# Kernel optimization log

Measured on AMD Instinct MI355X. Metric: run time of the kernel, lower is better.

Reference implementation:

```python
import jax, jax.numpy as jnp
import numpy as np


def setup_inputs() -> dict:
    key = jax.random.key(0)
    ks = jax.random.split(key, 5)
    B, S, D, H, K = 2, 2048, 1024, 16, 64
    std = 0.02
    return {
        "x": jax.random.normal(ks[0], (B, S, D), dtype=jnp.float32),
        "W_Q": jax.random.normal(ks[1], (H, D, K), dtype=jnp.float32) * std,
        "W_K": jax.random.normal(ks[2], (H, D, K), dtype=jnp.float32) * std,
        "W_V": jax.random.normal(ks[3], (H, D, K), dtype=jnp.float32) * std,
        "W_O": jax.random.normal(ks[4], (H, K, D), dtype=jnp.float32) * std,
        "b_Q": jnp.zeros((H, K), dtype=jnp.float32),
        "b_K": jnp.zeros((H, K), dtype=jnp.float32),
        "b_V": jnp.zeros((H, K), dtype=jnp.float32),
        "b_O": jnp.zeros((D,), dtype=jnp.float32),
    }


def reference(x, W_Q, W_K, W_V, W_O, b_Q, b_K, b_V, b_O):
    # x: (B, S, D); W_*: (H, D, K); W_O: (H, K, D)
    S = x.shape[1]
    d_head = W_Q.shape[-1]
    q = jnp.einsum('bpd,hdk->bphk', x, W_Q) + b_Q
    k = jnp.einsum('bpd,hdk->bphk', x, W_K) + b_K
    v = jnp.einsum('bpd,hdk->bphk', x, W_V) + b_V
    scores = jnp.einsum('bphk,bqhk->bhpq', q, k) / jnp.sqrt(jnp.float32(d_head))
    # causal mask: positions q > p (strict upper triangle) are masked
    causal = jnp.tril(jnp.ones((S, S), dtype=bool))
    scores = jnp.where(causal, scores, jnp.float32(-jnp.inf))
    pattern = jax.nn.softmax(scores, axis=-1)
    z = jnp.einsum('bhpq,bqhk->bphk', pattern, v)
    out = jnp.einsum('bphk,hkd->bpd', z, W_O) + b_O
    return out
```

## Files before the change

### kernel.cpp

```cpp
#include <hip/hip_runtime.h>

typedef unsigned short u16;
typedef __attribute__((ext_vector_type(4))) float f32x4;
typedef __attribute__((ext_vector_type(8))) short s16x8;
typedef __attribute__((ext_vector_type(4))) unsigned short u16x4;
typedef __attribute__((ext_vector_type(2))) unsigned int u32x2;

#define S_ 2048
#define D_ 1024
#define H_ 16
#define KH 64
#define M_ 4096
#define BH_ 32

__device__ __forceinline__ float bf2f(u16 v) {
    union { unsigned int u; float f; } x; x.u = ((unsigned int)v) << 16; return x.f;
}
__device__ __forceinline__ u16 f2bf(float f) {
    union { float ff; unsigned int u; } x; x.ff = f;
    unsigned int r = x.u + 0x7fffu + ((x.u >> 16) & 1u);
    return (u16)(r >> 16);
}
__device__ __forceinline__ unsigned int cvt_pk_bf16(float lo, float hi) {
    unsigned int d;
    asm("v_cvt_pk_bf16_f32 %0, %1, %2" : "=v"(d) : "v"(lo), "v"(hi));
    return d;
}

__global__ void kcvt_x(const float* __restrict__ x, u16* __restrict__ xb) {
    const int i = (blockIdx.x * 256 + threadIdx.x) * 4;
    const float4 v = *(const float4*)&x[i];
    u16x4 o;
    o.x = f2bf(v.x); o.y = f2bf(v.y); o.z = f2bf(v.z); o.w = f2bf(v.w);
    *(u16x4*)&xb[i] = o;
}

__global__ void ktrans_w(const float* __restrict__ WQ, const float* __restrict__ WK,
                         const float* __restrict__ WV, const float* __restrict__ WO,
                         u16* __restrict__ wt) {
    __shared__ u16 tile[64][65];
    const int mat = blockIdx.z;
    const float* src = (mat == 0) ? WQ : (mat == 1) ? WK : (mat == 2) ? WV : WO;
    u16* dst = wt + (size_t)mat * 1048576;
    const int a0 = blockIdx.x * 64, b0 = blockIdx.y * 64;
    const int t = threadIdx.x;
    const int bl = t & 63, ar = t >> 6;
    #pragma unroll
    for (int i = 0; i < 16; ++i) {
        int a = a0 + i * 4 + ar, b = b0 + bl;
        size_t sa = (mat < 3) ? (((size_t)(b >> 6)) << 16) + ((size_t)a << 6) + (b & 63)
                              : (size_t)a * 1024 + b;
        tile[i * 4 + ar][bl] = f2bf(src[sa]);
    }
    __syncthreads();
    #pragma unroll
    for (int i = 0; i < 16; ++i) {
        int bl2 = i * 4 + ar;
        dst[(size_t)(b0 + bl2) * 1024 + a0 + bl] = tile[bl][bl2];
    }
}

__global__ __launch_bounds__(256)
void kgemm0(const u16* __restrict__ A, const u16* __restrict__ Wt,
            const float* __restrict__ b0p, const float* __restrict__ b1p,
            const float* __restrict__ b2p,
            u16* __restrict__ Qo, u16* __restrict__ Ko, u16* __restrict__ Vto) {
    __shared__ u16 As[2][128 * 32];
    __shared__ u16 Bs[2][128 * 32];
    const int t = threadIdx.x;
    const int l = t & 63, w = t >> 6;
    const int lq = l & 15, lg = l >> 4;
    const int wr = w >> 1, wc = w & 1;
    const int m0 = blockIdx.x * 128;
    const int n0 = blockIdx.y * 128;
    const int z = blockIdx.z;
    const u16* Bt = Wt + (size_t)z * 1048576;
    const float* bias = (z == 0) ? b0p : (z == 1) ? b1p : b2p;

    f32x4 acc[4][4] = {};

    auto stage = [&](int kt, int buf) {
        #pragma unroll
        for (int i = 0; i < 2; ++i) {
            int idx = t + i * 256;
            int row = idx >> 2, cc = idx & 3;
            const u16* ga = A + (size_t)(m0 + row) * 1024 + kt * 32 + cc * 8;
            const u16* gb = Bt + (size_t)(n0 + row) * 1024 + kt * 32 + cc * 8;
            __builtin_amdgcn_global_load_lds(
                (const __attribute__((address_space(1))) unsigned int*)ga,
                (__attribute__((address_space(3))) unsigned int*)(&As[buf][idx * 8]),
                16, 0, 0);
            __builtin_amdgcn_global_load_lds(
                (const __attribute__((address_space(1))) unsigned int*)gb,
                (__attribute__((address_space(3))) unsigned int*)(&Bs[buf][idx * 8]),
                16, 0, 0);
        }
    };

    stage(0, 0);
    __syncthreads();
    for (int kt = 0; kt < 32; ++kt) {
        const int cur = kt & 1;
        if (kt + 1 < 32) stage(kt + 1, cur ^ 1);
        s16x8 af[4], bf[4];
        #pragma unroll
        for (int m = 0; m < 4; ++m)
            af[m] = *(const s16x8*)&As[cur][(wr * 64 + m * 16 + lq) * 32 + lg * 8];
        #pragma unroll
        for (int n = 0; n < 4; ++n)
            bf[n] = *(const s16x8*)&Bs[cur][(wc * 64 + n * 16 + lq) * 32 + lg * 8];
        #pragma unroll
        for (int m = 0; m < 4; ++m)
            #pragma unroll
            for (int n = 0; n < 4; ++n)
                acc[m][n] = __builtin_amdgcn_mfma_f32_16x16x32_bf16(
                    bf[n], af[m], acc[m][n], 0, 0, 0);
        __syncthreads();
    }

    #pragma unroll
    for (int n = 0; n < 4; ++n) {
        const int gcolb = n0 + wc * 64 + n * 16 + lg * 4;
        const float4 bv = *(const float4*)&bias[gcolb];
        const int h = gcolb >> 6, kk0 = gcolb & 63;
        #pragma unroll
        for (int m = 0; m < 4; ++m) {
            const int grow = m0 + wr * 64 + m * 16 + lq;
            const int b = grow >> 11, s = grow & 2047;
            const float v0 = acc[m][n][0] + bv.x;
            const float v1 = acc[m][n][1] + bv.y;
            const float v2 = acc[m][n][2] + bv.z;
            const float v3 = acc[m][n][3] + bv.w;
            if (z == 2) {
                u16* vb = Vto + ((size_t)((b * 16 + h) * 64 + kk0) * 2048 + s);
                vb[0] = f2bf(v0); vb[2048] = f2bf(v1);
                vb[4096] = f2bf(v2); vb[6144] = f2bf(v3);
            } else {
                u16* outp = (z == 0) ? Qo : Ko;
                u32x2 wp;
                wp.x = cvt_pk_bf16(v0, v1);
                wp.y = cvt_pk_bf16(v2, v3);
                *(u32x2*)&outp[((size_t)(b * 16 + h) * 2048 + s) * 64 + kk0] = wp;
            }
        }
    }
}

__global__ __launch_bounds__(256)
void kgemm1(const u16* __restrict__ A, const u16* __restrict__ Bt,
            const float* __restrict__ bias, float* __restrict__ fo) {
    __shared__ u16 As[2][128 * 32];
    __shared__ u16 Bs[2][64 * 32];
    const int t = threadIdx.x;
    const int l = t & 63, w = t >> 6;
    const int lq = l & 15, lg = l >> 4;
    const int wr = w >> 1, wc = w & 1;
    const int m0 = blockIdx.x * 128;
    const int n0 = blockIdx.y * 64;

    f32x4 acc[4][2] = {};

    auto stage = [&](int kt, int buf) {
        #pragma unroll
        for (int i = 0; i < 2; ++i) {
            int idx = t + i * 256;
            int row = idx >> 2, cc = idx & 3;
            __builtin_amdgcn_global_load_lds(
                (const __attribute__((address_space(1))) unsigned int*)
                    (A + (size_t)(m0 + row) * 1024 + kt * 32 + cc * 8),
                (__attribute__((address_space(3))) unsigned int*)(&As[buf][idx * 8]),
                16, 0, 0);
        }
        {
            int row = t >> 2, cc = t & 3;
            __builtin_amdgcn_global_load_lds(
                (const __attribute__((address_space(1))) unsigned int*)
                    (Bt + (size_t)(n0 + row) * 1024 + kt * 32 + cc * 8),
                (__attribute__((address_space(3))) unsigned int*)(&Bs[buf][t * 8]),
                16, 0, 0);
        }
    };

    stage(0, 0);
    __syncthreads();
    for (int kt = 0; kt < 32; ++kt) {
        const int cur = kt & 1;
        if (kt + 1 < 32) stage(kt + 1, cur ^ 1);
        s16x8 af[4], bf[2];
        #pragma unroll
        for (int m = 0; m < 4; ++m)
            af[m] = *(const s16x8*)&As[cur][(wr * 64 + m * 16 + lq) * 32 + lg * 8];
        #pragma unroll
        for (int n = 0; n < 2; ++n)
            bf[n] = *(const s16x8*)&Bs[cur][(wc * 32 + n * 16 + lq) * 32 + lg * 8];
        #pragma unroll
        for (int m = 0; m < 4; ++m)
            #pragma unroll
            for (int n = 0; n < 2; ++n)
                acc[m][n] = __builtin_amdgcn_mfma_f32_16x16x32_bf16(
                    bf[n], af[m], acc[m][n], 0, 0, 0);
        __syncthreads();
    }

    #pragma unroll
    for (int n = 0; n < 2; ++n) {
        const int gcolb = n0 + wc * 32 + n * 16 + lg * 4;
        const float4 bv = *(const float4*)&bias[gcolb];
        #pragma unroll
        for (int m = 0; m < 4; ++m) {
            const int grow = m0 + wr * 64 + m * 16 + lq;
            float4 o;
            o.x = acc[m][n][0] + bv.x;
            o.y = acc[m][n][1] + bv.y;
            o.z = acc[m][n][2] + bv.z;
            o.w = acc[m][n][3] + bv.w;
            *(float4*)&fo[(size_t)grow * 1024 + gcolb] = o;
        }
    }
}

__global__ __launch_bounds__(256)
void kattn(const u16* __restrict__ Q, const u16* __restrict__ K,
           const u16* __restrict__ Vt, u16* __restrict__ Z) {
    __shared__ u16 Ks[2][64 * 64];
    __shared__ u16 Vs[2][64 * 64];
    __shared__ u16 Pl[4][16 * 72];
    const int t = threadIdx.x, l = t & 63, w = t >> 6;
    const int lq = l & 15, lg = l >> 4;

    const int lin = blockIdx.x + 16 * blockIdx.y;
    const int xcd = lin & 7;
    const int idx = lin >> 3;
    const int pair = idx & 15;
    const int bh = xcd + 8 * (idx >> 4);

    const size_t base = (size_t)bh * (S_ * KH);
    const u16* Qb = Q + base;
    const u16* Kb = K + base;
    const u16* Vb = Vt + base;
    const int b = bh >> 4, h = bh & 15;
    u16* Pw = &Pl[w][0];

    const int c0 = ((lg ^ (lq & 7)) * 8);
    const int c1 = c0 ^ 32;
    const float NINF = -__builtin_inff();

    auto stage = [&](int k0, int buf) {
        #pragma unroll
        for (int i = 0; i < 2; ++i) {
            const int idx2 = t + i * 256;
            const int row = idx2 >> 3;
            const int cg = (idx2 & 7) ^ (row & 7);
            __builtin_amdgcn_global_load_lds(
                (const __attribute__((address_space(1))) unsigned int*)
                    (Kb + (size_t)(k0 + row) * KH + cg * 8),
                (__attribute__((address_space(3))) unsigned int*)(&Ks[buf][idx2 * 8]),
                16, 0, 0);
            __builtin_amdgcn_global_load_lds(
                (const __attribute__((address_space(1))) unsigned int*)
                    (Vb + (size_t)row * S_ + k0 + cg * 8),
                (__attribute__((address_space(3))) unsigned int*)(&Vs[buf][idx2 * 8]),
                16, 0, 0);
        }
    };

    const float SCL = 0.18033688011112042f;

    #pragma unroll 1
    for (int ph = 0; ph < 2; ++ph) {
        const int qt = ph ? (31 - pair) : pair;
        const int nt = qt + 1;
        const int qs = qt * 64 + w * 16;
        const int lim = w * 16 + lq;

        const s16x8 qf0 = *(const s16x8*)&Qb[(size_t)(qs + lq) * KH + lg * 8];
        const s16x8 qf1 = *(const s16x8*)&Qb[(size_t)(qs + lq) * KH + 32 + lg * 8];

        float mrow = NINF, lrow = 0.f;
        f32x4 zacc[4] = {};

        stage(0, 0);
        __syncthreads();

        for (int kt = 0; kt < nt; ++kt) {
            const int buf = kt & 1;
            if (kt + 1 < nt) stage((kt + 1) * 64, buf ^ 1);

            f32x4 sf[4] = {};
            __builtin_amdgcn_s_setprio(1);
            #pragma unroll
            for (int kf = 0; kf < 4; ++kf) {
                const int row = kf * 16 + lq;
                const s16x8 ka = *(const s16x8*)&Ks[buf][row * 64 + c0];
                const s16x8 kb = *(const s16x8*)&Ks[buf][row * 64 + c1];
                sf[kf] = __builtin_amdgcn_mfma_f32_16x16x32_bf16(ka, qf0, sf[kf], 0, 0, 0);
                sf[kf] = __builtin_amdgcn_mfma_f32_16x16x32_bf16(kb, qf1, sf[kf], 0, 0, 0);
            }
            __builtin_amdgcn_s_setprio(0);

            float p[4][4];
            const bool diag = (kt == qt);
            #pragma unroll
            for (int kf = 0; kf < 4; ++kf)
                #pragma unroll
                for (int r = 0; r < 4; ++r) {
                    float v = sf[kf][r] * SCL;
                    if (diag && (kf * 16 + lg * 4 + r) > lim) v = NINF;
                    p[kf][r] = v;
                }

            float mk[4];
            #pragma unroll
            for (int kf = 0; kf < 4; ++kf)
                mk[kf] = fmaxf(fmaxf(p[kf][0], p[kf][1]), fmaxf(p[kf][2], p[kf][3]));
            float tmax = fmaxf(fmaxf(mk[0], mk[1]), fmaxf(mk[2], mk[3]));
            tmax = fmaxf(tmax, __shfl_xor(tmax, 16));
            tmax = fmaxf(tmax, __shfl_xor(tmax, 32));

            float alpha = 1.f;
            if (!__all(tmax <= mrow + 8.f)) {
                const float nm = fmaxf(mrow, tmax);
                alpha = exp2f(mrow - nm);
                mrow = nm;
                #pragma unroll
                for (int nf = 0; nf < 4; ++nf)
                    #pragma unroll
                    for (int r = 0; r < 4; ++r)
                        zacc[nf][r] *= alpha;
            }

            float sk[4];
            #pragma unroll
            for (int kf = 0; kf < 4; ++kf) {
                #pragma unroll
                for (int r = 0; r < 4; ++r)
                    p[kf][r] = exp2f(p[kf][r] - mrow);
                sk[kf] = (p[kf][0] + p[kf][1]) + (p[kf][2] + p[kf][3]);
            }
            float rsum = (sk[0] + sk[1]) + (sk[2] + sk[3]);
            rsum += __shfl_xor(rsum, 16);
            rsum += __shfl_xor(rsum, 32);
            lrow = lrow * alpha + rsum;

            #pragma unroll
            for (int kf = 0; kf < 4; ++kf) {
                u32x2 wp;
                wp.x = cvt_pk_bf16(p[kf][0], p[kf][1]);
                wp.y = cvt_pk_bf16(p[kf][2], p[kf][3]);
                *(u32x2*)&Pw[lq * 72 + kf * 16 + lg * 4] = wp;
            }
            const s16x8 pa0 = *(const s16x8*)&Pw[lq * 72 + lg * 8];
            const s16x8 pa1 = *(const s16x8*)&Pw[lq * 72 + 32 + lg * 8];

            __builtin_amdgcn_s_setprio(1);
            #pragma unroll
            for (int nf = 0; nf < 4; ++nf) {
                const int row = nf * 16 + lq;
                const s16x8 v0 = *(const s16x8*)&Vs[buf][row * 64 + c0];
                const s16x8 v1 = *(const s16x8*)&Vs[buf][row * 64 + c1];
                zacc[nf] = __builtin_amdgcn_mfma_f32_16x16x32_bf16(v0, pa0, zacc[nf], 0, 0, 0);
                zacc[nf] = __builtin_amdgcn_mfma_f32_16x16x32_bf16(v1, pa1, zacc[nf], 0, 0, 0);
            }
            __builtin_amdgcn_s_setprio(0);
            __syncthreads();
        }

        const float rinv = 1.f / lrow;
        const size_t zrow = (size_t)(b * S_ + qs + lq) * 1024 + h * 64;
        #pragma unroll
        for (int nf = 0; nf < 4; ++nf) {
            u32x2 wp;
            wp.x = cvt_pk_bf16(zacc[nf][0] * rinv, zacc[nf][1] * rinv);
            wp.y = cvt_pk_bf16(zacc[nf][2] * rinv, zacc[nf][3] * rinv);
            *(u32x2*)&Z[zrow + nf * 16 + lg * 4] = wp;
        }
    }
}

extern "C" void kernel_launch(void* const* d_in, const int* in_sizes, int n_in,
                              void* d_out, int out_size, void* d_ws, size_t ws_size,
                              hipStream_t stream) {
    const float* x  = (const float*)d_in[0];
    const float* WQ = (const float*)d_in[1];
    const float* WK = (const float*)d_in[2];
    const float* WV = (const float*)d_in[3];
    const float* WO = (const float*)d_in[4];
    const float* bQ = (const float*)d_in[5];
    const float* bK = (const float*)d_in[6];
    const float* bV = (const float*)d_in[7];
    const float* bO = (const float*)d_in[8];
    float* out = (float*)d_out;

    u16* ws  = (u16*)d_ws;
    u16* xb  = ws;
    u16* wt  = xb + 4194304u;
    u16* Qb  = wt + 4194304u;
    u16* Kb  = Qb + 4194304u;
    u16* Vtb = Kb + 4194304u;
    u16* Zb  = Vtb + 4194304u;

    kcvt_x<<<dim3(4096), 256, 0, stream>>>(x, xb);
    ktrans_w<<<dim3(16, 16, 4), 256, 0, stream>>>(WQ, WK, WV, WO, wt);
    kgemm0<<<dim3(32, 8, 3), 256, 0, stream>>>(
        xb, wt, bQ, bK, bV, Qb, Kb, Vtb);
    kattn<<<dim3(16, BH_), 256, 0, stream>>>(Qb, Kb, Vtb, Zb);
    kgemm1<<<dim3(32, 16), 256, 0, stream>>>(
        Zb, wt + 3u * 1048576u, bO, out);
}
```

Baseline: 206.5 us.

## Software-pipeline QK^T into the previous step and vectorize V-transpose stores

The attention loop now computes the next tile's QK^T scores right after the barrier at the end of the current step, using ping-pong score registers, so the MFMA work for tile kt+1 can overlap the softmax of tile kt. Separately, the projection GEMM swaps MFMA operand order for the V output so each lane holds four consecutive sequence positions. That lets the transposed V store be one packed 8-byte write instead of four scalar 2-byte writes. The cost is extra registers for the second score buffer, which may reduce occupancy.

```diff
diff --git a/kernel.cpp b/kernel.cpp
--- a/kernel.cpp
+++ b/kernel.cpp
@@ -109,37 +109,54 @@
         #pragma unroll
         for (int n = 0; n < 4; ++n)
             bf[n] = *(const s16x8*)&Bs[cur][(wc * 64 + n * 16 + lq) * 32 + lg * 8];
-        #pragma unroll
-        for (int m = 0; m < 4; ++m)
-            #pragma unroll
-            for (int n = 0; n < 4; ++n)
-                acc[m][n] = __builtin_amdgcn_mfma_f32_16x16x32_bf16(
-                    bf[n], af[m], acc[m][n], 0, 0, 0);
+        if (z == 2) {
+            #pragma unroll
+            for (int m = 0; m < 4; ++m)
+                #pragma unroll
+                for (int n = 0; n < 4; ++n)
+                    acc[m][n] = __builtin_amdgcn_mfma_f32_16x16x32_bf16(
+                        af[m], bf[n], acc[m][n], 0, 0, 0);
+        } else {
+            #pragma unroll
+            for (int m = 0; m < 4; ++m)
+                #pragma unroll
+                for (int n = 0; n < 4; ++n)
+                    acc[m][n] = __builtin_amdgcn_mfma_f32_16x16x32_bf16(
+                        bf[n], af[m], acc[m][n], 0, 0, 0);
+        }
         __syncthreads();
     }
 
-    #pragma unroll
-    for (int n = 0; n < 4; ++n) {
-        const int gcolb = n0 + wc * 64 + n * 16 + lg * 4;
-        const float4 bv = *(const float4*)&bias[gcolb];
-        const int h = gcolb >> 6, kk0 = gcolb & 63;
-        #pragma unroll
-        for (int m = 0; m < 4; ++m) {
-            const int grow = m0 + wr * 64 + m * 16 + lq;
-            const int b = grow >> 11, s = grow & 2047;
-            const float v0 = acc[m][n][0] + bv.x;
-            const float v1 = acc[m][n][1] + bv.y;
-            const float v2 = acc[m][n][2] + bv.z;
-            const float v3 = acc[m][n][3] + bv.w;
-            if (z == 2) {
-                u16* vb = Vto + ((size_t)((b * 16 + h) * 64 + kk0) * 2048 + s);
-                vb[0] = f2bf(v0); vb[2048] = f2bf(v1);
-                vb[4096] = f2bf(v2); vb[6144] = f2bf(v3);
-            } else {
-                u16* outp = (z == 0) ? Qo : Ko;
+    if (z == 2) {
+        #pragma unroll
+        for (int n = 0; n < 4; ++n) {
+            const int gcol = n0 + wc * 64 + n * 16 + lq;
+            const float bv = bias[gcol];
+            const int h = gcol >> 6, kk = gcol & 63;
+            #pragma unroll
+            for (int m = 0; m < 4; ++m) {
+                const int growb = m0 + wr * 64 + m * 16 + lg * 4;
+                const int b = growb >> 11, s = growb & 2047;
                 u32x2 wp;
-                wp.x = cvt_pk_bf16(v0, v1);
-                wp.y = cvt_pk_bf16(v2, v3);
+                wp.x = cvt_pk_bf16(acc[m][n][0] + bv, acc[m][n][1] + bv);
+                wp.y = cvt_pk_bf16(acc[m][n][2] + bv, acc[m][n][3] + bv);
+                *(u32x2*)&Vto[(size_t)((b * 16 + h) * 64 + kk) * 2048 + s] = wp;
+            }
+        }
+    } else {
+        u16* outp = (z == 0) ? Qo : Ko;
+        #pragma unroll
+        for (int n = 0; n < 4; ++n) {
+            const int gcolb = n0 + wc * 64 + n * 16 + lg * 4;
+            const float4 bv = *(const float4*)&bias[gcolb];
+            const int h = gcolb >> 6, kk0 = gcolb & 63;
+            #pragma unroll
+            for (int m = 0; m < 4; ++m) {
+                const int grow = m0 + wr * 64 + m * 16 + lq;
+                const int b = grow >> 11, s = grow & 2047;
+                u32x2 wp;
+                wp.x = cvt_pk_bf16(acc[m][n][0] + bv.x, acc[m][n][1] + bv.y);
+                wp.y = cvt_pk_bf16(acc[m][n][2] + bv.z, acc[m][n][3] + bv.w);
                 *(u32x2*)&outp[((size_t)(b * 16 + h) * 2048 + s) * 64 + kk0] = wp;
             }
         }
@@ -244,6 +261,7 @@
     const int c0 = ((lg ^ (lq & 7)) * 8);
     const int c1 = c0 ^ 32;
     const float NINF = -__builtin_inff();
+    const float SCL = 0.18033688011112042f;
 
     auto stage = [&](int k0, int buf) {
         #pragma unroll
@@ -263,8 +281,6 @@
                 16, 0, 0);
         }
     };
-
-    const float SCL = 0.18033688011112042f;
 
     #pragma unroll 1
     for (int ph = 0; ph < 2; ++ph) {
@@ -278,25 +294,26 @@
 
         float mrow = NINF, lrow = 0.f;
         f32x4 zacc[4] = {};
-
-        stage(0, 0);
-        __syncthreads();
-
-        for (int kt = 0; kt < nt; ++kt) {
-            const int buf = kt & 1;
-            if (kt + 1 < nt) stage((kt + 1) * 64, buf ^ 1);
-
-            f32x4 sf[4] = {};
+        f32x4 sfA[4], sfB[4];
+
+        auto QK = [&](int buf, f32x4 (&sfo)[4]) {
             __builtin_amdgcn_s_setprio(1);
             #pragma unroll
             for (int kf = 0; kf < 4; ++kf) {
                 const int row = kf * 16 + lq;
                 const s16x8 ka = *(const s16x8*)&Ks[buf][row * 64 + c0];
                 const s16x8 kb = *(const s16x8*)&Ks[buf][row * 64 + c1];
-                sf[kf] = __builtin_amdgcn_mfma_f32_16x16x32_bf16(ka, qf0, sf[kf], 0, 0, 0);
-                sf[kf] = __builtin_amdgcn_mfma_f32_16x16x32_bf16(kb, qf1, sf[kf], 0, 0, 0);
+                f32x4 z4 = {};
+                z4 = __builtin_amdgcn_mfma_f32_16x16x32_bf16(ka, qf0, z4, 0, 0, 0);
+                sfo[kf] = __builtin_amdgcn_mfma_f32_16x16x32_bf16(kb, qf1, z4, 0, 0, 0);
             }
             __builtin_amdgcn_s_setprio(0);
+        };
+
+        auto STEP = [&](f32x4 (&sfc)[4], f32x4 (&sfn)[4], int kt) {
+            const int buf = kt & 1;
+            const bool hn = (kt + 1 < nt);
+            if (hn) stage((kt + 1) * 64, buf ^ 1);
 
             float p[4][4];
             const bool diag = (kt == qt);
@@ -304,7 +321,7 @@
             for (int kf = 0; kf < 4; ++kf)
                 #pragma unroll
                 for (int r = 0; r < 4; ++r) {
-                    float v = sf[kf][r] * SCL;
+                    float v = sfc[kf][r] * SCL;
                     if (diag && (kf * 16 + lg * 4 + r) > lim) v = NINF;
                     p[kf][r] = v;
                 }
@@ -363,6 +380,15 @@
             }
             __builtin_amdgcn_s_setprio(0);
             __syncthreads();
+            if (hn) QK(buf ^ 1, sfn);
+        };
+
+        stage(0, 0);
+        __syncthreads();
+        QK(0, sfA);
+        for (int kt = 0; kt < nt; kt += 2) {
+            STEP(sfA, sfB, kt);
+            if (kt + 1 < nt) STEP(sfB, sfA, kt + 1);
         }
 
         const float rinv = 1.f / lrow;
```

Measured after the change: 238.0 us. 15.3% more time.

## Split V projection into transposed-MFMA kernel and remap output GEMM blocks per XCD

Applied to the files above, without the earlier changes.

The QKV projection is split in two. Q and K keep the old kernel, while V gets a template variant that swaps the MFMA operands. The accumulator then holds consecutive sequence positions per lane, so the transposed V store becomes packed 8-byte writes instead of scattered 2-byte stores. The output projection GEMM also switches to a 1D grid with an XCD-aware block mapping so blocks sharing A rows land on the same die's L2. The cost is an extra kernel launch, and the smaller V-only grid may underfill the GPU.

```diff
diff --git a/kernel.cpp b/kernel.cpp
--- a/kernel.cpp
+++ b/kernel.cpp
@@ -60,11 +60,11 @@
     }
 }
 
+template <int VM>
 __global__ __launch_bounds__(256)
-void kgemm0(const u16* __restrict__ A, const u16* __restrict__ Wt,
-            const float* __restrict__ b0p, const float* __restrict__ b1p,
-            const float* __restrict__ b2p,
-            u16* __restrict__ Qo, u16* __restrict__ Ko, u16* __restrict__ Vto) {
+void kgemm0t(const u16* __restrict__ A, const u16* __restrict__ Wt,
+             const float* __restrict__ b0p, const float* __restrict__ b1p,
+             u16* __restrict__ o0, u16* __restrict__ o1) {
     __shared__ u16 As[2][128 * 32];
     __shared__ u16 Bs[2][128 * 32];
     const int t = threadIdx.x;
@@ -73,9 +73,10 @@
     const int wr = w >> 1, wc = w & 1;
     const int m0 = blockIdx.x * 128;
     const int n0 = blockIdx.y * 128;
-    const int z = blockIdx.z;
+    const int z = (VM == 0) ? blockIdx.z : 0;
     const u16* Bt = Wt + (size_t)z * 1048576;
-    const float* bias = (z == 0) ? b0p : (z == 1) ? b1p : b2p;
+    const float* bias = z ? b1p : b0p;
+    u16* outp = z ? o1 : o0;
 
     f32x4 acc[4][4] = {};
 
@@ -112,34 +113,46 @@
         #pragma unroll
         for (int m = 0; m < 4; ++m)
             #pragma unroll
-            for (int n = 0; n < 4; ++n)
-                acc[m][n] = __builtin_amdgcn_mfma_f32_16x16x32_bf16(
-                    bf[n], af[m], acc[m][n], 0, 0, 0);
+            for (int n = 0; n < 4; ++n) {
+                if constexpr (VM == 1)
+                    acc[m][n] = __builtin_amdgcn_mfma_f32_16x16x32_bf16(
+                        af[m], bf[n], acc[m][n], 0, 0, 0);
+                else
+                    acc[m][n] = __builtin_amdgcn_mfma_f32_16x16x32_bf16(
+                        bf[n], af[m], acc[m][n], 0, 0, 0);
+            }
         __syncthreads();
     }
 
-    #pragma unroll
-    for (int n = 0; n < 4; ++n) {
-        const int gcolb = n0 + wc * 64 + n * 16 + lg * 4;
-        const float4 bv = *(const float4*)&bias[gcolb];
-        const int h = gcolb >> 6, kk0 = gcolb & 63;
-        #pragma unroll
-        for (int m = 0; m < 4; ++m) {
-            const int grow = m0 + wr * 64 + m * 16 + lq;
-            const int b = grow >> 11, s = grow & 2047;
-            const float v0 = acc[m][n][0] + bv.x;
-            const float v1 = acc[m][n][1] + bv.y;
-            const float v2 = acc[m][n][2] + bv.z;
-            const float v3 = acc[m][n][3] + bv.w;
-            if (z == 2) {
-                u16* vb = Vto + ((size_t)((b * 16 + h) * 64 + kk0) * 2048 + s);
-                vb[0] = f2bf(v0); vb[2048] = f2bf(v1);
-                vb[4096] = f2bf(v2); vb[6144] = f2bf(v3);
-            } else {
-                u16* outp = (z == 0) ? Qo : Ko;
+    if constexpr (VM == 1) {
+        #pragma unroll
+        for (int n = 0; n < 4; ++n) {
+            const int gcol = n0 + wc * 64 + n * 16 + lq;
+            const float bv = bias[gcol];
+            const int h = gcol >> 6, kk = gcol & 63;
+            #pragma unroll
+            for (int m = 0; m < 4; ++m) {
+                const int growb = m0 + wr * 64 + m * 16 + lg * 4;
+                const int b = growb >> 11, s = growb & 2047;
                 u32x2 wp;
-                wp.x = cvt_pk_bf16(v0, v1);
-                wp.y = cvt_pk_bf16(v2, v3);
+                wp.x = cvt_pk_bf16(acc[m][n][0] + bv, acc[m][n][1] + bv);
+                wp.y = cvt_pk_bf16(acc[m][n][2] + bv, acc[m][n][3] + bv);
+                *(u32x2*)&o0[(size_t)((b * 16 + h) * 64 + kk) * 2048 + s] = wp;
+            }
+        }
+    } else {
+        #pragma unroll
+        for (int n = 0; n < 4; ++n) {
+            const int gcolb = n0 + wc * 64 + n * 16 + lg * 4;
+            const float4 bv = *(const float4*)&bias[gcolb];
+            const int h = gcolb >> 6, kk0 = gcolb & 63;
+            #pragma unroll
+            for (int m = 0; m < 4; ++m) {
+                const int grow = m0 + wr * 64 + m * 16 + lq;
+                const int b = grow >> 11, s = grow & 2047;
+                u32x2 wp;
+                wp.x = cvt_pk_bf16(acc[m][n][0] + bv.x, acc[m][n][1] + bv.y);
+                wp.y = cvt_pk_bf16(acc[m][n][2] + bv.z, acc[m][n][3] + bv.w);
                 *(u32x2*)&outp[((size_t)(b * 16 + h) * 2048 + s) * 64 + kk0] = wp;
             }
         }
@@ -155,8 +168,14 @@
     const int l = t & 63, w = t >> 6;
     const int lq = l & 15, lg = l >> 4;
     const int wr = w >> 1, wc = w & 1;
-    const int m0 = blockIdx.x * 128;
-    const int n0 = blockIdx.y * 64;
+
+    const int lin = blockIdx.x;
+    const int xcd = lin & 7;
+    const int s = lin >> 3;
+    const int nb = s & 15;
+    const int mb = (s >> 4) * 8 + xcd;
+    const int m0 = mb * 128;
+    const int n0 = nb * 64;
 
     f32x4 acc[4][2] = {};
 
@@ -401,9 +420,10 @@
 
     kcvt_x<<<dim3(4096), 256, 0, stream>>>(x, xb);
     ktrans_w<<<dim3(16, 16, 4), 256, 0, stream>>>(WQ, WK, WV, WO, wt);
-    kgemm0<<<dim3(32, 8, 3), 256, 0, stream>>>(
-        xb, wt, bQ, bK, bV, Qb, Kb, Vtb);
+    kgemm0t<0><<<dim3(32, 8, 2), 256, 0, stream>>>(xb, wt, bQ, bK, Qb, Kb);
+    kgemm0t<1><<<dim3(32, 8, 1), 256, 0, stream>>>(
+        xb, wt + 2u * 1048576u, bV, nullptr, Vtb, nullptr);
     kattn<<<dim3(16, BH_), 256, 0, stream>>>(Qb, Kb, Vtb, Zb);
-    kgemm1<<<dim3(32, 16), 256, 0, stream>>>(
+    kgemm1<<<dim3(512), 256, 0, stream>>>(
         Zb, wt + 3u * 1048576u, bO, out);
 }
```

Result: slower. 223.0 us (+8.0%).

## Launch one attention block per q-tile longest-first, XCD-aware swizzle for output GEMM

Applied to the files above, without the earlier changes.

Each attention block now handles a single 64-row query tile instead of a balanced pair, giving 1024 blocks ordered so the longest causal tiles are dispatched first. Block indices are mapped so blocks sharing a batch-head land on the same XCD. The output projection GEMM gets a 1D grid with an XCD-aware mapping so blocks reading the same A rows share an XCD's L2. This trades the paired-tile load balancing for more, smaller blocks and relies on the dispatch order to keep the tail short.

```diff
diff --git a/kernel.cpp b/kernel.cpp
--- a/kernel.cpp
+++ b/kernel.cpp
@@ -155,8 +155,14 @@
     const int l = t & 63, w = t >> 6;
     const int lq = l & 15, lg = l >> 4;
     const int wr = w >> 1, wc = w & 1;
-    const int m0 = blockIdx.x * 128;
-    const int n0 = blockIdx.y * 64;
+
+    const int lin = blockIdx.x;
+    const int xcd = lin & 7;
+    const int s = lin >> 3;
+    const int nb = s & 15;
+    const int mb = (s >> 4) * 8 + xcd;
+    const int m0 = mb * 128;
+    const int n0 = nb * 64;
 
     f32x4 acc[4][2] = {};
 
@@ -228,11 +234,11 @@
     const int t = threadIdx.x, l = t & 63, w = t >> 6;
     const int lq = l & 15, lg = l >> 4;
 
-    const int lin = blockIdx.x + 16 * blockIdx.y;
+    const int lin = blockIdx.x;
     const int xcd = lin & 7;
-    const int idx = lin >> 3;
-    const int pair = idx & 15;
-    const int bh = xcd + 8 * (idx >> 4);
+    const int r = lin >> 3;
+    const int qt = 31 - (r >> 2);
+    const int bh = xcd + 8 * (r & 3);
 
     const size_t base = (size_t)bh * (S_ * KH);
     const u16* Qb = Q + base;
@@ -244,6 +250,7 @@
     const int c0 = ((lg ^ (lq & 7)) * 8);
     const int c1 = c0 ^ 32;
     const float NINF = -__builtin_inff();
+    const float SCL = 0.18033688011112042f;
 
     auto stage = [&](int k0, int buf) {
         #pragma unroll
@@ -264,116 +271,110 @@
         }
     };
 
-    const float SCL = 0.18033688011112042f;
-
-    #pragma unroll 1
-    for (int ph = 0; ph < 2; ++ph) {
-        const int qt = ph ? (31 - pair) : pair;
-        const int nt = qt + 1;
-        const int qs = qt * 64 + w * 16;
-        const int lim = w * 16 + lq;
-
-        const s16x8 qf0 = *(const s16x8*)&Qb[(size_t)(qs + lq) * KH + lg * 8];
-        const s16x8 qf1 = *(const s16x8*)&Qb[(size_t)(qs + lq) * KH + 32 + lg * 8];
-
-        float mrow = NINF, lrow = 0.f;
-        f32x4 zacc[4] = {};
-
-        stage(0, 0);
+    const int nt = qt + 1;
+    const int qs = qt * 64 + w * 16;
+    const int lim = w * 16 + lq;
+
+    const s16x8 qf0 = *(const s16x8*)&Qb[(size_t)(qs + lq) * KH + lg * 8];
+    const s16x8 qf1 = *(const s16x8*)&Qb[(size_t)(qs + lq) * KH + 32 + lg * 8];
+
+    float mrow = NINF, lrow = 0.f;
+    f32x4 zacc[4] = {};
+
+    stage(0, 0);
+    __syncthreads();
+
+    for (int kt = 0; kt < nt; ++kt) {
+        const int buf = kt & 1;
+        if (kt + 1 < nt) stage((kt + 1) * 64, buf ^ 1);
+
+        f32x4 sf[4] = {};
+        __builtin_amdgcn_s_setprio(1);
+        #pragma unroll
+        for (int kf = 0; kf < 4; ++kf) {
+            const int row = kf * 16 + lq;
+            const s16x8 ka = *(const s16x8*)&Ks[buf][row * 64 + c0];
+            const s16x8 kb = *(const s16x8*)&Ks[buf][row * 64 + c1];
+            sf[kf] = __builtin_amdgcn_mfma_f32_16x16x32_bf16(ka, qf0, sf[kf], 0, 0, 0);
+            sf[kf] = __builtin_amdgcn_mfma_f32_16x16x32_bf16(kb, qf1, sf[kf], 0, 0, 0);
+        }
+        __builtin_amdgcn_s_setprio(0);
+
+        float p[4][4];
+        const bool diag = (kt == qt);
+        #pragma unroll
+        for (int kf = 0; kf < 4; ++kf)
+            #pragma unroll
+            for (int r2 = 0; r2 < 4; ++r2) {
+                float v = sf[kf][r2] * SCL;
+                if (diag && (kf * 16 + lg * 4 + r2) > lim) v = NINF;
+                p[kf][r2] = v;
+            }
+
+        float mk[4];
+        #pragma unroll
+        for (int kf = 0; kf < 4; ++kf)
+            mk[kf] = fmaxf(fmaxf(p[kf][0], p[kf][1]), fmaxf(p[kf][2], p[kf][3]));
+        float tmax = fmaxf(fmaxf(mk[0], mk[1]), fmaxf(mk[2], mk[3]));
+        tmax = fmaxf(tmax, __shfl_xor(tmax, 16));
+        tmax = fmaxf(tmax, __shfl_xor(tmax, 32));
+
+        float alpha = 1.f;
+        if (!__all(tmax <= mrow + 8.f)) {
+            const float nm = fmaxf(mrow, tmax);
+            alpha = exp2f(mrow - nm);
+            mrow = nm;
+            #pragma unroll
+            for (int nf = 0; nf < 4; ++nf)
+                #pragma unroll
+                for (int r2 = 0; r2 < 4; ++r2)
+                    zacc[nf][r2] *= alpha;
+        }
+
+        float sk[4];
+        #pragma unroll
+        for (int kf = 0; kf < 4; ++kf) {
+            #pragma unroll
+            for (int r2 = 0; r2 < 4; ++r2)
+                p[kf][r2] = exp2f(p[kf][r2] - mrow);
+            sk[kf] = (p[kf][0] + p[kf][1]) + (p[kf][2] + p[kf][3]);
+        }
+        float rsum = (sk[0] + sk[1]) + (sk[2] + sk[3]);
+        rsum += __shfl_xor(rsum, 16);
+        rsum += __shfl_xor(rsum, 32);
+        lrow = lrow * alpha + rsum;
+
+        #pragma unroll
+        for (int kf = 0; kf < 4; ++kf) {
+            u32x2 wp;
+            wp.x = cvt_pk_bf16(p[kf][0], p[kf][1]);
+            wp.y = cvt_pk_bf16(p[kf][2], p[kf][3]);
+            *(u32x2*)&Pw[lq * 72 + kf * 16 + lg * 4] = wp;
+        }
+        const s16x8 pa0 = *(const s16x8*)&Pw[lq * 72 + lg * 8];
+        const s16x8 pa1 = *(const s16x8*)&Pw[lq * 72 + 32 + lg * 8];
+
+        __builtin_amdgcn_s_setprio(1);
+        #pragma unroll
+        for (int nf = 0; nf < 4; ++nf) {
+            const int row = nf * 16 + lq;
+            const s16x8 v0 = *(const s16x8*)&Vs[buf][row * 64 + c0];
+            const s16x8 v1 = *(const s16x8*)&Vs[buf][row * 64 + c1];
+            zacc[nf] = __builtin_amdgcn_mfma_f32_16x16x32_bf16(v0, pa0, zacc[nf], 0, 0, 0);
+            zacc[nf] = __builtin_amdgcn_mfma_f32_16x16x32_bf16(v1, pa1, zacc[nf], 0, 0, 0);
+        }
+        __builtin_amdgcn_s_setprio(0);
         __syncthreads();
-
-        for (int kt = 0; kt < nt; ++kt) {
-            const int buf = kt & 1;
-            if (kt + 1 < nt) stage((kt + 1) * 64, buf ^ 1);
-
-            f32x4 sf[4] = {};
-            __builtin_amdgcn_s_setprio(1);
-            #pragma unroll
-            for (int kf = 0; kf < 4; ++kf) {
-                const int row = kf * 16 + lq;
-                const s16x8 ka = *(const s16x8*)&Ks[buf][row * 64 + c0];
-                const s16x8 kb = *(const s16x8*)&Ks[buf][row * 64 + c1];
-                sf[kf] = __builtin_amdgcn_mfma_f32_16x16x32_bf16(ka, qf0, sf[kf], 0, 0, 0);
-                sf[kf] = __builtin_amdgcn_mfma_f32_16x16x32_bf16(kb, qf1, sf[kf], 0, 0, 0);
-            }
-            __builtin_amdgcn_s_setprio(0);
-
-            float p[4][4];
-            const bool diag = (kt == qt);
-            #pragma unroll
-            for (int kf = 0; kf < 4; ++kf)
-                #pragma unroll
-                for (int r = 0; r < 4; ++r) {
-                    float v = sf[kf][r] * SCL;
-                    if (diag && (kf * 16 + lg * 4 + r) > lim) v = NINF;
-                    p[kf][r] = v;
-                }
-
-            float mk[4];
-            #pragma unroll
-            for (int kf = 0; kf < 4; ++kf)
-                mk[kf] = fmaxf(fmaxf(p[kf][0], p[kf][1]), fmaxf(p[kf][2], p[kf][3]));
-            float tmax = fmaxf(fmaxf(mk[0], mk[1]), fmaxf(mk[2], mk[3]));
-            tmax = fmaxf(tmax, __shfl_xor(tmax, 16));
-            tmax = fmaxf(tmax, __shfl_xor(tmax, 32));
-
-            float alpha = 1.f;
-            if (!__all(tmax <= mrow + 8.f)) {
-                const float nm = fmaxf(mrow, tmax);
-                alpha = exp2f(mrow - nm);
-                mrow = nm;
-                #pragma unroll
-                for (int nf = 0; nf < 4; ++nf)
-                    #pragma unroll
-                    for (int r = 0; r < 4; ++r)
-                        zacc[nf][r] *= alpha;
-            }
-
-            float sk[4];
-            #pragma unroll
-            for (int kf = 0; kf < 4; ++kf) {
-                #pragma unroll
-                for (int r = 0; r < 4; ++r)
-                    p[kf][r] = exp2f(p[kf][r] - mrow);
-                sk[kf] = (p[kf][0] + p[kf][1]) + (p[kf][2] + p[kf][3]);
-            }
-            float rsum = (sk[0] + sk[1]) + (sk[2] + sk[3]);
-            rsum += __shfl_xor(rsum, 16);
-            rsum += __shfl_xor(rsum, 32);
-            lrow = lrow * alpha + rsum;
-
-            #pragma unroll
-            for (int kf = 0; kf < 4; ++kf) {
-                u32x2 wp;
-                wp.x = cvt_pk_bf16(p[kf][0], p[kf][1]);
-                wp.y = cvt_pk_bf16(p[kf][2], p[kf][3]);
-                *(u32x2*)&Pw[lq * 72 + kf * 16 + lg * 4] = wp;
-            }
-            const s16x8 pa0 = *(const s16x8*)&Pw[lq * 72 + lg * 8];
-            const s16x8 pa1 = *(const s16x8*)&Pw[lq * 72 + 32 + lg * 8];
-
-            __builtin_amdgcn_s_setprio(1);
-            #pragma unroll
-            for (int nf = 0; nf < 4; ++nf) {
-                const int row = nf * 16 + lq;
-                const s16x8 v0 = *(const s16x8*)&Vs[buf][row * 64 + c0];
-                const s16x8 v1 = *(const s16x8*)&Vs[buf][row * 64 + c1];
-                zacc[nf] = __builtin_amdgcn_mfma_f32_16x16x32_bf16(v0, pa0, zacc[nf], 0, 0, 0);
-                zacc[nf] = __builtin_amdgcn_mfma_f32_16x16x32_bf16(v1, pa1, zacc[nf], 0, 0, 0);
-            }
-            __builtin_amdgcn_s_setprio(0);
-            __syncthreads();
-        }
-
-        const float rinv = 1.f / lrow;
-        const size_t zrow = (size_t)(b * S_ + qs + lq) * 1024 + h * 64;
-        #pragma unroll
-        for (int nf = 0; nf < 4; ++nf) {
-            u32x2 wp;
-            wp.x = cvt_pk_bf16(zacc[nf][0] * rinv, zacc[nf][1] * rinv);
-            wp.y = cvt_pk_bf16(zacc[nf][2] * rinv, zacc[nf][3] * rinv);
-            *(u32x2*)&Z[zrow + nf * 16 + lg * 4] = wp;
-        }
+    }
+
+    const float rinv = 1.f / lrow;
+    const size_t zrow = (size_t)(b * S_ + qs + lq) * 1024 + h * 64;
+    #pragma unroll
+    for (int nf = 0; nf < 4; ++nf) {
+        u32x2 wp;
+        wp.x = cvt_pk_bf16(zacc[nf][0] * rinv, zacc[nf][1] * rinv);
+        wp.y = cvt_pk_bf16(zacc[nf][2] * rinv, zacc[nf][3] * rinv);
+        *(u32x2*)&Z[zrow + nf * 16 + lg * 4] = wp;
     }
 }
 
@@ -403,7 +404,7 @@
     ktrans_w<<<dim3(16, 16, 4), 256, 0, stream>>>(WQ, WK, WV, WO, wt);
     kgemm0<<<dim3(32, 8, 3), 256, 0, stream>>>(
         xb, wt, bQ, bK, bV, Qb, Kb, Vtb);
-    kattn<<<dim3(16, BH_), 256, 0, stream>>>(Qb, Kb, Vtb, Zb);
-    kgemm1<<<dim3(32, 16), 256, 0, stream>>>(
+    kattn<<<dim3(1024), 256, 0, stream>>>(Qb, Kb, Vtb, Zb);
+    kgemm1<<<dim3(512), 256, 0, stream>>>(
         Zb, wt + 3u * 1048576u, bO, out);
 }
```

New measurement: 199.8 us. -3.2%, faster.
